# Kernel tuning notes

Measured on AMD Instinct MI355X. Metric: run time of the kernel, lower is better.

Reference implementation:

```python
import jax, jax.numpy as jnp
import numpy as np

MERSENNE_P = (1 << 31) - 1  # prime used by universal hashing


def _uhash_cols(random_numbers, n_full_cols, n_comp_cols):
    """Universal-hash map from full-weight column index -> compressed column index.
    h(j) = ((r0*j + r1) mod P) mod n_comp_cols  (ints stay well within int64).
    """
    j = jnp.arange(n_full_cols, dtype=jnp.int64)
    r0 = random_numbers[0]
    r1 = random_numbers[1]
    return ((r0 * j + r1) % MERSENNE_P) % n_comp_cols


def setup_inputs() -> dict:
    key = jax.random.key(0)
    k1, k2, k3 = jax.random.split(key, 3)
    in_features, out_features, redn_factor = 8192, 8192, 4
    init_scale = 1.0 / np.sqrt(in_features)
    x = jax.random.normal(k1, (64, in_features), dtype=jnp.float32)
    weight = jax.random.uniform(
        k2, (out_features, in_features // redn_factor), dtype=jnp.float32,
        minval=-init_scale, maxval=init_scale)
    random_numbers = jax.random.randint(k3, (4,), 1, 1048576, dtype=jnp.int64)
    return {"x": x, "weight": weight, "random_numbers": random_numbers,
            "redn_factor": 4}


def reference(x, weight, random_numbers, redn_factor):
    # x: [..., K]; weight (compressed): [N, K // redn_factor]
    orig_shape = x.shape
    K = orig_shape[-1]
    x2d = x.reshape(-1, K)                      # preprocess: flatten leading dims
    n_comp = weight.shape[1]
    col_idx = _uhash_cols(random_numbers, K, n_comp)   # [K] hashed gather indices
    w_full = weight[:, col_idx]                 # [N, K] expanded via hashed gather
    y = x2d @ w_full.T                          # [rows, N]
    return y.reshape(*orig_shape[:-1], y.shape[-1])  # postprocess
```

## Files before the change

kernel.cpp:

```cpp
#include <hip/hip_runtime.h>
#include <hip/hip_bf16.h>

#define K_FULL   8192
#define M_ROWS   64
#define N_OUT    8192
#define N_COMP   2048
#define P_MERS   2147483647


typedef __attribute__((ext_vector_type(8))) short bf16x8;
typedef __attribute__((ext_vector_type(4))) float f32x4;

__device__ __forceinline__ short f2bfs(float f) {
    __hip_bfloat16 h = __float2bfloat16(f);
    return *reinterpret_cast<short*>(&h);
}

__device__ __forceinline__ int hash_col(int j, int rn0, int rn1, int rn2, int rn3) {
    if (rn1 == 0 && rn3 == 0) {
        unsigned long long xx = (unsigned long long)(unsigned int)rn0 * (unsigned int)j
                              + (unsigned long long)(unsigned int)rn2;
        unsigned long long t = (xx & (unsigned long long)P_MERS) + (xx >> 31);
        if (t >= (unsigned long long)P_MERS) t -= (unsigned long long)P_MERS;
        return (int)(t & (N_COMP - 1));
    } else {
        unsigned int t = (unsigned int)rn0 * (unsigned int)j + (unsigned int)rn1;
        int ti = (int)t;
        int m1 = ti % P_MERS;
        if (m1 < 0) m1 += P_MERS;
        return m1 & (N_COMP - 1);
    }
}

__global__ __launch_bounds__(512) void k_part(const float* __restrict__ x,
                                              const int* __restrict__ rn,
                                              float* __restrict__ partial) {
    __shared__ float row[N_COMP];
    const int b = blockIdx.x;
    const int m = b >> 2;
    const int jq = b & 3;
    const int tid = threadIdx.x;
#pragma unroll
    for (int i = 0; i < 4; ++i) row[tid + 512 * i] = 0.0f;
    const int rn0 = rn[0], rn1 = rn[1], rn2 = rn[2], rn3 = rn[3];
    __syncthreads();

    const int j0 = jq * 2048 + tid * 4;
    float4 v = *(const float4*)(x + (size_t)m * K_FULL + j0);
    atomicAdd(&row[hash_col(j0 + 0, rn0, rn1, rn2, rn3)], v.x);
    atomicAdd(&row[hash_col(j0 + 1, rn0, rn1, rn2, rn3)], v.y);
    atomicAdd(&row[hash_col(j0 + 2, rn0, rn1, rn2, rn3)], v.z);
    atomicAdd(&row[hash_col(j0 + 3, rn0, rn1, rn2, rn3)], v.w);
    __syncthreads();

    float4 o = { row[4 * tid], row[4 * tid + 1], row[4 * tid + 2], row[4 * tid + 3] };
    *(float4*)(partial + (size_t)b * N_COMP + 4 * tid) = o;
}

__global__ __launch_bounds__(256) void k_pack(const float* __restrict__ partial,
                                              unsigned short* __restrict__ xcB) {
    const int b = blockIdx.x;
    const int m = b >> 2;
    const int c0 = (b & 3) * 512 + threadIdx.x * 2;
    const float* p = partial + (size_t)m * 4 * N_COMP + c0;
    float s0 = p[0] + p[N_COMP] + p[2 * N_COMP] + p[3 * N_COMP];
    float s1 = p[1] + p[N_COMP + 1] + p[2 * N_COMP + 1] + p[3 * N_COMP + 1];
    unsigned int pk = (unsigned int)(unsigned short)f2bfs(s0)
                    | ((unsigned int)(unsigned short)f2bfs(s1) << 16);
    ((unsigned int*)(xcB + (size_t)m * N_COMP))[c0 >> 1] = pk;
}

#define KSLICES 8
#define KSL     (N_COMP / KSLICES)
#define KSTEPS  (KSL / 32)

__global__ __launch_bounds__(512) void k_gemm(const float* __restrict__ W,
                                              const unsigned short* __restrict__ xcB,
                                              float* __restrict__ y) {
    __shared__ float ys[KSLICES][M_ROWS][16];
    const int tid  = threadIdx.x;
    const int lane = tid & 63;
    const int w    = __builtin_amdgcn_readfirstlane(tid >> 6);
    const int nr   = lane & 15;
    const int kg   = lane >> 4;
    const int n0   = blockIdx.x * 16;

    const float*          wp = W   + (size_t)(n0 + nr) * N_COMP + w * KSL + kg * 8;
    const unsigned short* ap = xcB + (size_t)nr * N_COMP        + w * KSL + kg * 8;

    f32x4 acc0 = {0.f, 0.f, 0.f, 0.f};
    f32x4 acc1 = {0.f, 0.f, 0.f, 0.f};
    f32x4 acc2 = {0.f, 0.f, 0.f, 0.f};
    f32x4 acc3 = {0.f, 0.f, 0.f, 0.f};

#define LOADW(W0, W1, S) do { int ko_ = (S) * 32;                      \
        (W0) = *(const float4*)(wp + ko_);                             \
        (W1) = *(const float4*)(wp + ko_ + 4); } while (0)
#define LOADA(A0, A1, A2, A3, S) do { int ko_ = (S) * 32;              \
        (A0) = *(const bf16x8*)(ap + ko_);                             \
        (A1) = *(const bf16x8*)(ap + 16 * N_COMP + ko_);               \
        (A2) = *(const bf16x8*)(ap + 32 * N_COMP + ko_);               \
        (A3) = *(const bf16x8*)(ap + 48 * N_COMP + ko_); } while (0)
#define DOMFMA(W0, W1, A0, A1, A2, A3) do { bf16x8 b_;                 \
        b_[0] = f2bfs((W0).x); b_[1] = f2bfs((W0).y);                  \
        b_[2] = f2bfs((W0).z); b_[3] = f2bfs((W0).w);                  \
        b_[4] = f2bfs((W1).x); b_[5] = f2bfs((W1).y);                  \
        b_[6] = f2bfs((W1).z); b_[7] = f2bfs((W1).w);                  \
        acc0 = __builtin_amdgcn_mfma_f32_16x16x32_bf16((A0), b_, acc0, 0, 0, 0); \
        acc1 = __builtin_amdgcn_mfma_f32_16x16x32_bf16((A1), b_, acc1, 0, 0, 0); \
        acc2 = __builtin_amdgcn_mfma_f32_16x16x32_bf16((A2), b_, acc2, 0, 0, 0); \
        acc3 = __builtin_amdgcn_mfma_f32_16x16x32_bf16((A3), b_, acc3, 0, 0, 0); } while (0)

    float4 wa0, wa1, wb0, wb1;
    bf16x8 aa0, aa1, aa2, aa3, ab0, ab1, ab2, ab3;

    LOADW(wa0, wa1, 0);
    LOADA(aa0, aa1, aa2, aa3, 0);
#pragma unroll 1
    for (int s = 0; s < KSTEPS - 2; s += 2) {
        LOADW(wb0, wb1, s + 1);
        LOADA(ab0, ab1, ab2, ab3, s + 1);
        DOMFMA(wa0, wa1, aa0, aa1, aa2, aa3);
        LOADW(wa0, wa1, s + 2);
        LOADA(aa0, aa1, aa2, aa3, s + 2);
        DOMFMA(wb0, wb1, ab0, ab1, ab2, ab3);
    }
    LOADW(wb0, wb1, KSTEPS - 1);
    LOADA(ab0, ab1, ab2, ab3, KSTEPS - 1);
    DOMFMA(wa0, wa1, aa0, aa1, aa2, aa3);
    DOMFMA(wb0, wb1, ab0, ab1, ab2, ab3);

#pragma unroll
    for (int j = 0; j < 4; ++j) {
        ys[w][ 0 + kg * 4 + j][nr] = acc0[j];
        ys[w][16 + kg * 4 + j][nr] = acc1[j];
        ys[w][32 + kg * 4 + j][nr] = acc2[j];
        ys[w][48 + kg * 4 + j][nr] = acc3[j];
    }
    __syncthreads();

#pragma unroll
    for (int i = 0; i < 2; ++i) {
        int o = tid + 512 * i;
        int m = o >> 4;
        int n = o & 15;
        float s = 0.f;
#pragma unroll
        for (int q = 0; q < KSLICES; ++q) s += ys[q][m][n];
        y[(size_t)m * N_OUT + n0 + n] = s;
    }
}

extern "C" void kernel_launch(void* const* d_in, const int* in_sizes, int n_in,
                              void* d_out, int out_size, void* d_ws, size_t ws_size,
                              hipStream_t stream) {
    const float* x = (const float*)d_in[0];
    const float* W = (const float*)d_in[1];
    const int* rn  = (const int*)d_in[2];
    float* y       = (float*)d_out;

    float* partial      = (float*)d_ws;
    unsigned short* xcB = (unsigned short*)((char*)d_ws + 256 * N_COMP * sizeof(float));

    k_part<<<256, 512, 0, stream>>>(x, rn, partial);
    k_pack<<<256, 256, 0, stream>>>(partial, xcB);
    k_gemm<<<N_OUT / 16, 512, 0, stream>>>(W, xcB, y);
}
```

Measured before the change: 36.24 us.

## Fuse hash-scatter and bf16 pack into one kernel with MFMA-fragment layout

Merges the partial-sum scatter kernel and the pack kernel into a single per-row kernel (64 blocks of 1024 threads), which drops the fp32 partial buffer round trip and one launch. The compressed activation is written in a pre-swizzled fragment order so each GEMM lane does one contiguous 16-byte load. The GEMM's K split also changes from contiguous slices to interleaved 32-wide steps across warps. The cost is that the first stage now runs on only 64 blocks, which lowers parallelism there.

```diff
diff --git a/kernel.cpp b/kernel.cpp
--- a/kernel.cpp
+++ b/kernel.cpp
@@ -32,52 +32,44 @@
     }
 }
 
-__global__ __launch_bounds__(512) void k_part(const float* __restrict__ x,
-                                              const int* __restrict__ rn,
-                                              float* __restrict__ partial) {
+__global__ __launch_bounds__(1024) void k_xc(const float* __restrict__ x,
+                                             const int* __restrict__ rn,
+                                             unsigned int* __restrict__ xcF) {
     __shared__ float row[N_COMP];
-    const int b = blockIdx.x;
-    const int m = b >> 2;
-    const int jq = b & 3;
+    const int m = blockIdx.x;
     const int tid = threadIdx.x;
-#pragma unroll
-    for (int i = 0; i < 4; ++i) row[tid + 512 * i] = 0.0f;
+    row[tid] = 0.0f;
+    row[tid + 1024] = 0.0f;
     const int rn0 = rn[0], rn1 = rn[1], rn2 = rn[2], rn3 = rn[3];
     __syncthreads();
 
-    const int j0 = jq * 2048 + tid * 4;
-    float4 v = *(const float4*)(x + (size_t)m * K_FULL + j0);
-    atomicAdd(&row[hash_col(j0 + 0, rn0, rn1, rn2, rn3)], v.x);
-    atomicAdd(&row[hash_col(j0 + 1, rn0, rn1, rn2, rn3)], v.y);
-    atomicAdd(&row[hash_col(j0 + 2, rn0, rn1, rn2, rn3)], v.z);
-    atomicAdd(&row[hash_col(j0 + 3, rn0, rn1, rn2, rn3)], v.w);
+    const float* xm = x + (size_t)m * K_FULL;
+#pragma unroll
+    for (int it = 0; it < 2; ++it) {
+        int j0 = tid * 4 + it * 4096;
+        float4 v = *(const float4*)(xm + j0);
+        atomicAdd(&row[hash_col(j0 + 0, rn0, rn1, rn2, rn3)], v.x);
+        atomicAdd(&row[hash_col(j0 + 1, rn0, rn1, rn2, rn3)], v.y);
+        atomicAdd(&row[hash_col(j0 + 2, rn0, rn1, rn2, rn3)], v.z);
+        atomicAdd(&row[hash_col(j0 + 3, rn0, rn1, rn2, rn3)], v.w);
+    }
     __syncthreads();
 
-    float4 o = { row[4 * tid], row[4 * tid + 1], row[4 * tid + 2], row[4 * tid + 3] };
-    *(float4*)(partial + (size_t)b * N_COMP + 4 * tid) = o;
+    const int c0 = 2 * tid;
+    const int s  = c0 >> 5;
+    const int kg = (c0 >> 3) & 3;
+    const int e0 = c0 & 7;
+    const int g  = m >> 4;
+    const int nr = m & 15;
+    unsigned int pk = (unsigned int)(unsigned short)f2bfs(row[c0])
+                    | ((unsigned int)(unsigned short)f2bfs(row[c0 + 1]) << 16);
+    xcF[(((s * 4 + g) * 64 + kg * 16 + nr) << 2) + (e0 >> 1)] = pk;
 }
 
-__global__ __launch_bounds__(256) void k_pack(const float* __restrict__ partial,
-                                              unsigned short* __restrict__ xcB) {
-    const int b = blockIdx.x;
-    const int m = b >> 2;
-    const int c0 = (b & 3) * 512 + threadIdx.x * 2;
-    const float* p = partial + (size_t)m * 4 * N_COMP + c0;
-    float s0 = p[0] + p[N_COMP] + p[2 * N_COMP] + p[3 * N_COMP];
-    float s1 = p[1] + p[N_COMP + 1] + p[2 * N_COMP + 1] + p[3 * N_COMP + 1];
-    unsigned int pk = (unsigned int)(unsigned short)f2bfs(s0)
-                    | ((unsigned int)(unsigned short)f2bfs(s1) << 16);
-    ((unsigned int*)(xcB + (size_t)m * N_COMP))[c0 >> 1] = pk;
-}
-
-#define KSLICES 8
-#define KSL     (N_COMP / KSLICES)
-#define KSTEPS  (KSL / 32)
-
 __global__ __launch_bounds__(512) void k_gemm(const float* __restrict__ W,
-                                              const unsigned short* __restrict__ xcB,
+                                              const unsigned short* __restrict__ xcF,
                                               float* __restrict__ y) {
-    __shared__ float ys[KSLICES][M_ROWS][16];
+    __shared__ float ys[8][M_ROWS][16];
     const int tid  = threadIdx.x;
     const int lane = tid & 63;
     const int w    = __builtin_amdgcn_readfirstlane(tid >> 6);
@@ -85,22 +77,23 @@
     const int kg   = lane >> 4;
     const int n0   = blockIdx.x * 16;
 
-    const float*          wp = W   + (size_t)(n0 + nr) * N_COMP + w * KSL + kg * 8;
-    const unsigned short* ap = xcB + (size_t)nr * N_COMP        + w * KSL + kg * 8;
+    const float* wp = W + (size_t)(n0 + nr) * N_COMP + w * 32 + kg * 8;
+    const unsigned short* ap = xcF + (size_t)w * 2048 + lane * 8;
 
     f32x4 acc0 = {0.f, 0.f, 0.f, 0.f};
     f32x4 acc1 = {0.f, 0.f, 0.f, 0.f};
     f32x4 acc2 = {0.f, 0.f, 0.f, 0.f};
     f32x4 acc3 = {0.f, 0.f, 0.f, 0.f};
 
-#define LOADW(W0, W1, S) do { int ko_ = (S) * 32;                      \
-        (W0) = *(const float4*)(wp + ko_);                             \
-        (W1) = *(const float4*)(wp + ko_ + 4); } while (0)
-#define LOADA(A0, A1, A2, A3, S) do { int ko_ = (S) * 32;              \
-        (A0) = *(const bf16x8*)(ap + ko_);                             \
-        (A1) = *(const bf16x8*)(ap + 16 * N_COMP + ko_);               \
-        (A2) = *(const bf16x8*)(ap + 32 * N_COMP + ko_);               \
-        (A3) = *(const bf16x8*)(ap + 48 * N_COMP + ko_); } while (0)
+#define LOADW(W0, W1, T) do { int o_ = (T) * 256;                      \
+        (W0) = *(const float4*)(wp + o_);                              \
+        (W1) = *(const float4*)(wp + o_ + 4); } while (0)
+#define LOADA(A0, A1, A2, A3, T) do {                                  \
+        const unsigned short* p_ = ap + (size_t)(T) * 16384;           \
+        (A0) = *(const bf16x8*)(p_);                                   \
+        (A1) = *(const bf16x8*)(p_ + 512);                             \
+        (A2) = *(const bf16x8*)(p_ + 1024);                            \
+        (A3) = *(const bf16x8*)(p_ + 1536); } while (0)
 #define DOMFMA(W0, W1, A0, A1, A2, A3) do { bf16x8 b_;                 \
         b_[0] = f2bfs((W0).x); b_[1] = f2bfs((W0).y);                  \
         b_[2] = f2bfs((W0).z); b_[3] = f2bfs((W0).w);                  \
@@ -117,16 +110,16 @@
     LOADW(wa0, wa1, 0);
     LOADA(aa0, aa1, aa2, aa3, 0);
 #pragma unroll 1
-    for (int s = 0; s < KSTEPS - 2; s += 2) {
-        LOADW(wb0, wb1, s + 1);
-        LOADA(ab0, ab1, ab2, ab3, s + 1);
+    for (int t = 0; t < 6; t += 2) {
+        LOADW(wb0, wb1, t + 1);
+        LOADA(ab0, ab1, ab2, ab3, t + 1);
         DOMFMA(wa0, wa1, aa0, aa1, aa2, aa3);
-        LOADW(wa0, wa1, s + 2);
-        LOADA(aa0, aa1, aa2, aa3, s + 2);
+        LOADW(wa0, wa1, t + 2);
+        LOADA(aa0, aa1, aa2, aa3, t + 2);
         DOMFMA(wb0, wb1, ab0, ab1, ab2, ab3);
     }
-    LOADW(wb0, wb1, KSTEPS - 1);
-    LOADA(ab0, ab1, ab2, ab3, KSTEPS - 1);
+    LOADW(wb0, wb1, 7);
+    LOADA(ab0, ab1, ab2, ab3, 7);
     DOMFMA(wa0, wa1, aa0, aa1, aa2, aa3);
     DOMFMA(wb0, wb1, ab0, ab1, ab2, ab3);
 
@@ -146,7 +139,7 @@
         int n = o & 15;
         float s = 0.f;
 #pragma unroll
-        for (int q = 0; q < KSLICES; ++q) s += ys[q][m][n];
+        for (int q = 0; q < 8; ++q) s += ys[q][m][n];
         y[(size_t)m * N_OUT + n0 + n] = s;
     }
 }
@@ -159,10 +152,8 @@
     const int* rn  = (const int*)d_in[2];
     float* y       = (float*)d_out;
 
-    float* partial      = (float*)d_ws;
-    unsigned short* xcB = (unsigned short*)((char*)d_ws + 256 * N_COMP * sizeof(float));
+    unsigned int* xcF = (unsigned int*)d_ws;
 
-    k_part<<<256, 512, 0, stream>>>(x, rn, partial);
-    k_pack<<<256, 256, 0, stream>>>(partial, xcB);
-    k_gemm<<<N_OUT / 16, 512, 0, stream>>>(W, xcB, y);
+    k_xc<<<M_ROWS, 1024, 0, stream>>>(x, rn, xcF);
+    k_gemm<<<N_OUT / 16, 512, 0, stream>>>(W, (const unsigned short*)xcF, y);
 }
```

Result: faster. 34.30 us (-5.4%).
